# Kernel optimization log

Measured on AMD Instinct MI355X. Metric: run time of the kernel, lower is better.

## Reference

```python
import jax, jax.numpy as jnp
import numpy as np

EPS = 1e-6
INPUT_SIZE = 64
NUM_LEAVES = INPUT_SIZE
NUM_LAYERS = NUM_LEAVES - 1
BATCH = 262144
SINKHORN_ITERS = 20


def _clip01(v):
    return jnp.clip(v, EPS, 1.0 - EPS)


def _F_base(x, y, a, w0, w1):
    # Branches of F for a in [0.5, 2] (the non-recursive region), selected branchlessly.
    x = _clip01(x)
    y = _clip01(y)
    lin = w0 * x + w1 * y
    p = jnp.sqrt(3.0 / jnp.maximum(2.0 - a, EPS)) - 1.0
    g = (x ** (2.0 * w0) * y ** (2.0 * w1)) ** p
    rule0 = jnp.where((jnp.abs(x - 1.0) < EPS) & (jnp.abs(y - 1.0) < EPS), 1.0, 0.0)
    return jnp.where(
        jnp.abs(a - 2.0) < EPS, rule0,
        jnp.where(a >= 0.75, g,
                  jnp.where(a > 0.5, (3.0 - 4.0 * a) * lin + (4.0 * a - 2.0) * g, lin)))


def _F(x, y, a, w0, w1):
    # Full generalized_gcd F with the single-level De Morgan reflection for a < 0.5.
    x = _clip01(x)
    y = _clip01(y)
    hi = _F_base(x, y, a, w0, w1)
    a_ref = jnp.clip(1.0 - a, -1.0 + EPS, 2.0 - EPS)
    lo = 1.0 - _F_base(1.0 - x, 1.0 - y, a_ref, w0, w1)
    lin = w0 * x + w1 * y
    return jnp.where(jnp.abs(a - 0.5) < EPS, lin, jnp.where(a < 0.5, lo, hi))


def _sinkhorn(logits, n_iter=SINKHORN_ITERS):
    # Log-space Sinkhorn normalization -> (approximately) doubly-stochastic P.
    l = logits
    for _ in range(n_iter):
        l = l - jax.nn.logsumexp(l, axis=1, keepdims=True)
        l = l - jax.nn.logsumexp(l, axis=0, keepdims=True)
    return jnp.exp(l)


def setup_inputs() -> dict:
    key = jax.random.key(0)
    k1, k2, k3, k4 = jax.random.split(key, 4)
    x = jax.random.uniform(k1, (BATCH, INPUT_SIZE), dtype=jnp.float32)
    logits = jax.random.normal(k2, (INPUT_SIZE, NUM_LEAVES), dtype=jnp.float32)
    weights = jax.random.uniform(k3, (NUM_LAYERS,), dtype=jnp.float32)
    biases = jax.random.uniform(k4, (NUM_LAYERS,), dtype=jnp.float32)
    return {"x": x, "logits": logits, "weights": weights, "biases": biases}


def reference(x, logits, weights, biases):
    P = _sinkhorn(logits)                 # [INPUT_SIZE, NUM_LEAVES], columns sum to 1
    leaves = (x @ P).T                    # [NUM_LEAVES, BATCH]

    def step(carry, inp):
        leaf, w, b = inp
        nres = _F(carry, leaf, b, w, 1.0 - w)
        nres = jnp.where(jnp.isnan(nres), b, nres)  # NaN fallback to bias, as in torch forward
        return nres, None

    # Left-leaning tree: state_0 = leaf_0; state_i = F(state_{i-1}, leaf_i, b, w, 1-w)
    final, _ = jax.lax.scan(step, leaves[0], (leaves[1:], weights, biases))
    return final[:, None]                 # [BATCH, 1]
```

## Files before the change

### kernel.cpp

```cpp
#include <hip/hip_runtime.h>
#include <hip/hip_bf16.h>
#include <math.h>

#define EPS 1e-6f
#define N 64
#define NLAYERS 63
#define SINK_ITERS 20
#define LOG2E 1.4426950408889634f

typedef __attribute__((ext_vector_type(8))) short bf16x8;
typedef __attribute__((ext_vector_type(4))) float f32x4;

__device__ __forceinline__ unsigned short f2bf(float f) {
  unsigned int u = __float_as_uint(f);
  return (unsigned short)((u + 0x7FFFu + ((u >> 16) & 1u)) >> 16);
}

__global__ __launch_bounds__(64) void sinkhorn_kernel(
    const float* __restrict__ logits,
    const float* __restrict__ weights,
    const float* __restrict__ biases,
    unsigned short* __restrict__ Pfrag,
    float* __restrict__ layers) {
  __shared__ float T[64 * 65 + 128];
  const int l = threadIdx.x;

  float K[64];
  {
    const float4* lr = (const float4*)(logits + (l << 6));
    #pragma unroll
    for (int q = 0; q < 16; ++q) {
      float4 t = lr[q];
      K[4*q+0] = exp2f(t.x * LOG2E);
      K[4*q+1] = exp2f(t.y * LOG2E);
      K[4*q+2] = exp2f(t.z * LOG2E);
      K[4*q+3] = exp2f(t.w * LOG2E);
    }
  }
  #pragma unroll
  for (int j = 0; j < 64; ++j) T[l * 65 + j] = K[j];
  __syncthreads();
  float KT[64];
  #pragma unroll
  for (int k = 0; k < 64; ++k) KT[k] = T[k * 65 + l];
  __syncthreads();

  float* Uv = &T[64 * 65];
  float* Vv = &T[64 * 65 + 64];
  Vv[l] = 1.0f;
  __syncthreads();

  float u = 1.0f;
  for (int it = 0; it < SINK_ITERS; ++it) {
    float r = 0.f;
    #pragma unroll
    for (int j = 0; j < 64; ++j) r = fmaf(K[j], Vv[j], r);
    u = 1.0f / r;
    __syncthreads();
    Uv[l] = u;
    __syncthreads();
    float c = 0.f;
    #pragma unroll
    for (int k = 0; k < 64; ++k) c = fmaf(KT[k], Uv[k], c);
    float v = 1.0f / c;
    __syncthreads();
    Vv[l] = v;
    __syncthreads();
  }

  #pragma unroll
  for (int j = 0; j < 64; ++j) T[l * 65 + j] = u * K[j] * Vv[j];
  __syncthreads();

  #pragma unroll
  for (int s = 0; s < 2; ++s)
    #pragma unroll
    for (int t = 0; t < 4; ++t) {
      unsigned short buf[8];
      #pragma unroll
      for (int j = 0; j < 8; ++j)
        buf[j] = f2bf(T[(s*32 + ((l >> 4) << 3) + j) * 65 + t*16 + (l & 15)]);
      *(bf16x8*)(Pfrag + (((s*4 + t) * 64 + l) << 3)) = *(bf16x8*)buf;
    }

  if (l < NLAYERS) {
    float w0 = weights[l];
    float w1 = 1.0f - w0;
    float a  = biases[l];
    float e0 = 0.f, e1 = 0.f, cl = 0.f, cg = 0.f, mode;
    if (fabsf(a - 0.5f) < EPS) {
      mode = 0.0f;
    } else {
      float ae;
      if (a < 0.5f) { mode = 2.0f; ae = fminf(fmaxf(1.0f - a, -1.0f + EPS), 2.0f - EPS); }
      else          { mode = 1.0f; ae = a; }
      float pp = sqrtf(3.0f / fmaxf(2.0f - ae, EPS)) - 1.0f;
      if (ae >= 0.75f) { cl = 0.0f;            cg = 1.0f; }
      else             { cl = 3.0f - 4.0f*ae;  cg = 4.0f*ae - 2.0f; }
      e0 = 2.0f * w0 * pp;
      e1 = 2.0f * w1 * pp;
    }
    float* Lr = layers + l * 8;
    Lr[0] = w0; Lr[1] = w1; Lr[2] = e0; Lr[3] = e1;
    Lr[4] = cl; Lr[5] = cg; Lr[6] = a;  Lr[7] = mode;
  }
}

__device__ __forceinline__ float F_step(float st, float leaf,
                                        const float* __restrict__ Lp) {
  float w0 = Lp[0], w1 = Lp[1], e0 = Lp[2], e1 = Lp[3];
  float cl = Lp[4], cg = Lp[5], av = Lp[6], mf = Lp[7];
  float xx = fminf(fmaxf(st,   EPS), 1.0f - EPS);
  float yy = fminf(fmaxf(leaf, EPS), 1.0f - EPS);
  float r;
  if (mf < 0.5f) {
    r = w0 * xx + w1 * yy;
  } else {
    if (mf > 1.5f) { xx = 1.0f - xx; yy = 1.0f - yy; }
    float lin = w0 * xx + w1 * yy;
    float g   = exp2f(e0 * log2f(xx) + e1 * log2f(yy));
    r = cl * lin + cg * g;
    if (mf > 1.5f) r = 1.0f - r;
  }
  return (r != r) ? av : r;
}

__global__ __launch_bounds__(256, 4) void scan_kernel(
    const float* __restrict__ x,
    const unsigned short* __restrict__ Pfrag,
    const float* __restrict__ layers,
    float* __restrict__ out) {
  __shared__ __align__(16) unsigned char SM[256 * 72 * 2];
  unsigned short* Xs = (unsigned short*)SM;
  float* Lv = (float*)SM;
  const int tid = threadIdx.x;
  const int w = tid >> 6, l = tid & 63;
  const size_t rowbase = (size_t)blockIdx.x << 8;

  bf16x8 B[2][4];
  #pragma unroll
  for (int s = 0; s < 2; ++s)
    #pragma unroll
    for (int t = 0; t < 4; ++t)
      B[s][t] = *(const bf16x8*)(Pfrag + (((s*4 + t) * 64 + l) << 3));

  {
    const float4* xp = (const float4*)(x + (rowbase << 6));
    #pragma unroll
    for (int c = 0; c < 16; ++c) {
      int idx = (c << 8) + tid;
      float4 v = xp[idx];
      union { unsigned short us[4]; uint2 u2; } pk;
      pk.us[0] = f2bf(v.x); pk.us[1] = f2bf(v.y);
      pk.us[2] = f2bf(v.z); pk.us[3] = f2bf(v.w);
      int row = idx >> 4, cs = (idx & 15) << 2;
      *(uint2*)&Xs[row * 72 + cs] = pk.u2;
    }
  }
  __syncthreads();

  bf16x8 A[4][2];
  #pragma unroll
  for (int i = 0; i < 4; ++i)
    #pragma unroll
    for (int s = 0; s < 2; ++s)
      A[i][s] = *(bf16x8*)&Xs[(((w << 2) + i) * 16 + (l & 15)) * 72
                              + (s << 5) + ((l >> 4) << 3)];
  __syncthreads();

  float st;
  #pragma unroll
  for (int half = 0; half < 2; ++half) {
    #pragma unroll
    for (int i = 0; i < 4; ++i) {
      const int drow0 = ((w << 2) + i) * 16 + ((l >> 4) << 2);
      #pragma unroll
      for (int tn = 0; tn < 2; ++tn) {
        const int t = (half << 1) + tn;
        f32x4 acc = {0.f, 0.f, 0.f, 0.f};
        acc = __builtin_amdgcn_mfma_f32_16x16x32_bf16(A[i][0], B[0][t], acc, 0, 0, 0);
        acc = __builtin_amdgcn_mfma_f32_16x16x32_bf16(A[i][1], B[1][t], acc, 0, 0, 0);
        const int dcol = (tn << 4) + (l & 15);
        #pragma unroll
        for (int r = 0; r < 4; ++r)
          Lv[(drow0 + r) * 33 + dcol] = acc[r];
      }
    }
    __syncthreads();

    if (half == 0) {
      st = Lv[tid * 33];
      #pragma unroll
      for (int j = 1; j < 32; ++j)
        st = F_step(st, Lv[tid * 33 + j], layers + (j - 1) * 8);
    } else {
      #pragma unroll
      for (int j = 32; j < 64; ++j)
        st = F_step(st, Lv[tid * 33 + (j - 32)], layers + (j - 1) * 8);
    }
    __syncthreads();
  }

  out[rowbase + tid] = st;
}

extern "C" void kernel_launch(void* const* d_in, const int* in_sizes, int n_in,
                              void* d_out, int out_size, void* d_ws, size_t ws_size,
                              hipStream_t stream) {
  const float* x       = (const float*)d_in[0];
  const float* logits  = (const float*)d_in[1];
  const float* weights = (const float*)d_in[2];
  const float* biases  = (const float*)d_in[3];
  float* out = (float*)d_out;

  unsigned short* Pfrag = (unsigned short*)d_ws;
  float* layers = (float*)((char*)d_ws + 8 * 64 * 8 * sizeof(unsigned short));

  const int batch = out_size;

  hipLaunchKernelGGL(sinkhorn_kernel, dim3(1), dim3(64), 0, stream,
                     logits, weights, biases, Pfrag, layers);
  hipLaunchKernelGGL(scan_kernel, dim3(batch / 256), dim3(256), 0, stream,
                     x, Pfrag, layers, out);
}
```

Measured before the change: 133.6 us.

## Load x fragments directly into registers and drop block barriers in scan

The scan kernel now loads each lane's MFMA A-fragment straight from global memory and converts it to bf16 in registers. This removes the shared-memory staging pass and its two block-wide barriers. Each wave now writes and reads only its own 64-row slice of the leaf buffer, so the barriers around the matmul and scan phases are dropped and waves can run independently. The Sinkhorn kernel also switches to float4 shared-memory reads with four partial accumulators. The trade-off is global loads that are less coalesced (scattered 32-byte chunks per lane) in exchange for fewer barriers and less LDS traffic.

```diff
diff --git a/kernel.cpp b/kernel.cpp
--- a/kernel.cpp
+++ b/kernel.cpp
@@ -47,22 +47,36 @@
 
   float* Uv = &T[64 * 65];
   float* Vv = &T[64 * 65 + 64];
+  const float4* Uv4 = (const float4*)Uv;
+  const float4* Vv4 = (const float4*)Vv;
   Vv[l] = 1.0f;
   __syncthreads();
 
   float u = 1.0f;
   for (int it = 0; it < SINK_ITERS; ++it) {
-    float r = 0.f;
-    #pragma unroll
-    for (int j = 0; j < 64; ++j) r = fmaf(K[j], Vv[j], r);
-    u = 1.0f / r;
+    float s0 = 0.f, s1 = 0.f, s2 = 0.f, s3 = 0.f;
+    #pragma unroll
+    for (int q = 0; q < 16; ++q) {
+      float4 v = Vv4[q];
+      s0 = fmaf(K[4*q+0], v.x, s0);
+      s1 = fmaf(K[4*q+1], v.y, s1);
+      s2 = fmaf(K[4*q+2], v.z, s2);
+      s3 = fmaf(K[4*q+3], v.w, s3);
+    }
+    u = 1.0f / ((s0 + s1) + (s2 + s3));
     __syncthreads();
     Uv[l] = u;
     __syncthreads();
-    float c = 0.f;
-    #pragma unroll
-    for (int k = 0; k < 64; ++k) c = fmaf(KT[k], Uv[k], c);
-    float v = 1.0f / c;
+    float c0 = 0.f, c1 = 0.f, c2 = 0.f, c3 = 0.f;
+    #pragma unroll
+    for (int q = 0; q < 16; ++q) {
+      float4 uu = Uv4[q];
+      c0 = fmaf(KT[4*q+0], uu.x, c0);
+      c1 = fmaf(KT[4*q+1], uu.y, c1);
+      c2 = fmaf(KT[4*q+2], uu.z, c2);
+      c3 = fmaf(KT[4*q+3], uu.w, c3);
+    }
+    float v = 1.0f / ((c0 + c1) + (c2 + c3));
     __syncthreads();
     Vv[l] = v;
     __syncthreads();
@@ -76,11 +90,11 @@
   for (int s = 0; s < 2; ++s)
     #pragma unroll
     for (int t = 0; t < 4; ++t) {
-      unsigned short buf[8];
+      union { unsigned short us[8]; bf16x8 v; } buf;
       #pragma unroll
       for (int j = 0; j < 8; ++j)
-        buf[j] = f2bf(T[(s*32 + ((l >> 4) << 3) + j) * 65 + t*16 + (l & 15)]);
-      *(bf16x8*)(Pfrag + (((s*4 + t) * 64 + l) << 3)) = *(bf16x8*)buf;
+        buf.us[j] = f2bf(T[(s*32 + ((l >> 4) << 3) + j) * 65 + t*16 + (l & 15)]);
+      *(bf16x8*)(Pfrag + (((s*4 + t) * 64 + l) << 3)) = buf.v;
     }
 
   if (l < NLAYERS) {
@@ -130,13 +144,23 @@
     const unsigned short* __restrict__ Pfrag,
     const float* __restrict__ layers,
     float* __restrict__ out) {
-  __shared__ __align__(16) unsigned char SM[256 * 72 * 2];
-  unsigned short* Xs = (unsigned short*)SM;
-  float* Lv = (float*)SM;
+  __shared__ float Lv[256 * 33];
   const int tid = threadIdx.x;
   const int w = tid >> 6, l = tid & 63;
   const size_t rowbase = (size_t)blockIdx.x << 8;
 
+  float4 araw[4][2][2];
+  #pragma unroll
+  for (int i = 0; i < 4; ++i) {
+    const float* rp = x + (rowbase + (w << 6) + (i << 4) + (l & 15)) * 64
+                        + ((l >> 4) << 3);
+    #pragma unroll
+    for (int s = 0; s < 2; ++s) {
+      araw[i][s][0] = *(const float4*)(rp + (s << 5));
+      araw[i][s][1] = *(const float4*)(rp + (s << 5) + 4);
+    }
+  }
+
   bf16x8 B[2][4];
   #pragma unroll
   for (int s = 0; s < 2; ++s)
@@ -144,36 +168,26 @@
     for (int t = 0; t < 4; ++t)
       B[s][t] = *(const bf16x8*)(Pfrag + (((s*4 + t) * 64 + l) << 3));
 
-  {
-    const float4* xp = (const float4*)(x + (rowbase << 6));
-    #pragma unroll
-    for (int c = 0; c < 16; ++c) {
-      int idx = (c << 8) + tid;
-      float4 v = xp[idx];
-      union { unsigned short us[4]; uint2 u2; } pk;
-      pk.us[0] = f2bf(v.x); pk.us[1] = f2bf(v.y);
-      pk.us[2] = f2bf(v.z); pk.us[3] = f2bf(v.w);
-      int row = idx >> 4, cs = (idx & 15) << 2;
-      *(uint2*)&Xs[row * 72 + cs] = pk.u2;
-    }
-  }
-  __syncthreads();
-
   bf16x8 A[4][2];
   #pragma unroll
   for (int i = 0; i < 4; ++i)
     #pragma unroll
-    for (int s = 0; s < 2; ++s)
-      A[i][s] = *(bf16x8*)&Xs[(((w << 2) + i) * 16 + (l & 15)) * 72
-                              + (s << 5) + ((l >> 4) << 3)];
-  __syncthreads();
-
-  float st;
+    for (int s = 0; s < 2; ++s) {
+      union { unsigned short us[8]; bf16x8 v; } buf;
+      float4 v0 = araw[i][s][0], v1 = araw[i][s][1];
+      buf.us[0] = f2bf(v0.x); buf.us[1] = f2bf(v0.y);
+      buf.us[2] = f2bf(v0.z); buf.us[3] = f2bf(v0.w);
+      buf.us[4] = f2bf(v1.x); buf.us[5] = f2bf(v1.y);
+      buf.us[6] = f2bf(v1.z); buf.us[7] = f2bf(v1.w);
+      A[i][s] = buf.v;
+    }
+
+  float st = 0.f;
   #pragma unroll
   for (int half = 0; half < 2; ++half) {
     #pragma unroll
     for (int i = 0; i < 4; ++i) {
-      const int drow0 = ((w << 2) + i) * 16 + ((l >> 4) << 2);
+      const int drow0 = (w << 6) + (i << 4) + ((l >> 4) << 2);
       #pragma unroll
       for (int tn = 0; tn < 2; ++tn) {
         const int t = (half << 1) + tn;
@@ -186,8 +200,6 @@
           Lv[(drow0 + r) * 33 + dcol] = acc[r];
       }
     }
-    __syncthreads();
-
     if (half == 0) {
       st = Lv[tid * 33];
       #pragma unroll
@@ -198,7 +210,6 @@
       for (int j = 32; j < 64; ++j)
         st = F_step(st, Lv[tid * 33 + (j - 32)], layers + (j - 1) * 8);
     }
-    __syncthreads();
   }
 
   out[rowbase + tid] = st;
```

After: 132.3 us. About the same (-1.0%).
